# Kernel tuning notes

Measured on AMD Instinct MI355X. Metric: run time of the kernel, lower is better.

The kernel has to match this reference:

```python
import jax, jax.numpy as jnp
import numpy as np

N, E, T = 50000, 800000, 12
H, HEADS, L, O = 128, 4, 3, 12
C = H // HEADS
NEG_SLOPE = 0.2
LN_EPS = 1e-5


def setup_inputs() -> dict:
    key = jax.random.key(0)
    ks = iter(jax.random.split(key, 32))
    rn = lambda shape, s=0.1: jax.random.normal(next(ks), shape, jnp.float32) * s
    return {
        "x": rn((N, T), 1.0),
        "edge_index": jax.random.randint(next(ks), (2, E), 0, N, dtype=jnp.int32),
        "edge_attr": jax.random.uniform(next(ks), (E, 1), jnp.float32),
        "gru_Wih0": rn((3 * H, 1)), "gru_Whh0": rn((3 * H, H)),
        "gru_bih0": rn((3 * H,)), "gru_bhh0": rn((3 * H,)),
        "gru_Wih1": rn((3 * H, H)), "gru_Whh1": rn((3 * H, H)),
        "gru_bih1": rn((3 * H,)), "gru_bhh1": rn((3 * H,)),
        "gat_Wl": rn((L, H, H)), "gat_bl": rn((L, H)),
        "gat_Wr": rn((L, H, H)), "gat_br": rn((L, H)),
        "gat_We": rn((L, 1, H)),
        "gat_att": rn((L, HEADS, C)),
        "gat_bias": rn((L, H)),
        "ln_gamma": jnp.ones((L, H), jnp.float32),
        "ln_beta": jnp.zeros((L, H), jnp.float32),
        "fc_W1": rn((H, H)), "fc_b1": rn((H,)),
        "fc_W2": rn((H, O)), "fc_b2": rn((O,)),
    }


def _gru_layer(xs, Wih, Whh, bih, bhh):
    # xs: [T, N, D] time-major. Standard torch GRU cell math.
    gx = jnp.einsum('tnd,gd->tng', xs, Wih) + bih  # [T, N, 3H]
    h0 = jnp.zeros((xs.shape[1], H), xs.dtype)

    def step(h, g):
        gh = h @ Whh.T + bhh
        r = jax.nn.sigmoid(g[:, :H] + gh[:, :H])
        z = jax.nn.sigmoid(g[:, H:2 * H] + gh[:, H:2 * H])
        n = jnp.tanh(g[:, 2 * H:] + r * gh[:, 2 * H:])
        h_new = (1.0 - z) * n + z * h
        return h_new, h_new

    hT, hs = jax.lax.scan(step, h0, gx)
    return hT, hs


def _gatv2(x, src, dst, edge_attr, Wl, bl, Wr, br, We, att, bias):
    # GATv2Conv with edge features, no self loops, concat heads.
    xl = (x @ Wl + bl).reshape(N, HEADS, C)   # source transform (x_j)
    xr = (x @ Wr + br).reshape(N, HEADS, C)   # target transform (x_i)
    ee = (edge_attr @ We).reshape(-1, HEADS, C)
    m = xl[src] + xr[dst] + ee                # [E, HEADS, C]
    s = jnp.sum(jax.nn.leaky_relu(m, NEG_SLOPE) * att, axis=-1)  # [E, HEADS]
    smax = jax.lax.stop_gradient(jax.ops.segment_max(s, dst, num_segments=N))
    es = jnp.exp(s - smax[dst])
    denom = jax.ops.segment_sum(es, dst, num_segments=N)
    alpha = es / jnp.maximum(denom[dst], 1e-16)
    out = jax.ops.segment_sum(alpha[:, :, None] * xl[src], dst, num_segments=N)
    return out.reshape(N, H) + bias


def _layernorm(x, g, b):
    mu = jnp.mean(x, -1, keepdims=True)
    var = jnp.var(x, -1, keepdims=True)
    return (x - mu) * jax.lax.rsqrt(var + LN_EPS) * g + b


def _forward(x, edge_index, edge_attr,
             gru_Wih0, gru_Whh0, gru_bih0, gru_bhh0,
             gru_Wih1, gru_Whh1, gru_bih1, gru_bhh1,
             gat_Wl, gat_bl, gat_Wr, gat_br, gat_We, gat_att, gat_bias,
             ln_gamma, ln_beta, fc_W1, fc_b1, fc_W2, fc_b2):
    # Temporal: 2-layer GRU over the window, take final hidden of top layer.
    xs = x.T[:, :, None]                                  # [T, N, 1]
    _, hs0 = _gru_layer(xs, gru_Wih0, gru_Whh0, gru_bih0, gru_bhh0)
    h, _ = _gru_layer(hs0, gru_Wih1, gru_Whh1, gru_bih1, gru_bhh1)  # [N, H]

    src, dst = edge_index[0], edge_index[1]
    for l in range(L):
        res = h
        z = _gatv2(h, src, dst, edge_attr,
                   gat_Wl[l], gat_bl[l], gat_Wr[l], gat_br[l],
                   gat_We[l], gat_att[l], gat_bias[l])
        z = _layernorm(z, ln_gamma[l], ln_beta[l])
        h = jax.nn.elu(z) + res                           # dropout off (eval)

    h1 = jax.nn.relu(h @ fc_W1 + fc_b1)
    return h1 @ fc_W2 + fc_b2                             # [N, O]


def reference(x, edge_index, edge_attr,
              gru_Wih0, gru_Whh0, gru_bih0, gru_bhh0,
              gru_Wih1, gru_Whh1, gru_bih1, gru_bhh1,
              gat_Wl, gat_bl, gat_Wr, gat_br, gat_We, gat_att, gat_bias,
              ln_gamma, ln_beta, fc_W1, fc_b1, fc_W2, fc_b2):
    return _forward(x, edge_index, edge_attr,
                    gru_Wih0, gru_Whh0, gru_bih0, gru_bhh0,
                    gru_Wih1, gru_Whh1, gru_bih1, gru_bhh1,
                    gat_Wl, gat_bl, gat_Wr, gat_br, gat_We, gat_att, gat_bias,
                    ln_gamma, ln_beta, fc_W1, fc_b1, fc_W2, fc_b2)
```

## Files before the change

### kernel.cpp

```cpp
#include <hip/hip_runtime.h>

#define NN 50000
#define EE 800000
#define TT 12
#define HH 128
#define LLAYERS 3
#define OO 12

typedef __attribute__((ext_vector_type(8))) short short8;
typedef __attribute__((ext_vector_type(4))) float float4v;
typedef unsigned short ushort_t;

#define MFMA_BF16 __builtin_amdgcn_mfma_f32_16x16x32_bf16

#define L2E  1.4426950408889634f
#define L2E2 2.8853900817779268f

#if __has_builtin(__builtin_amdgcn_exp2f)
#define EXP2(x) __builtin_amdgcn_exp2f(x)
#else
#define EXP2(x) __expf((x) * 0.6931471805599453f)
#endif

__device__ __forceinline__ ushort_t f2b(float f) {
    union { float f; unsigned u; } v; v.f = f;
    unsigned u = v.u;
    return (ushort_t)((u + 0x7FFFu + ((u >> 16) & 1u)) >> 16);
}
__device__ __forceinline__ float b2f(ushort_t b) {
    union { unsigned u; float f; } v; v.u = ((unsigned)b) << 16; return v.f;
}
__device__ __forceinline__ short8 ld8(const ushort_t* p) { return *(const short8*)p; }

__device__ __forceinline__ float rcpf_(float x) { return __builtin_amdgcn_rcpf(x); }
__device__ __forceinline__ float sig2(float y) { return rcpf_(1.f + EXP2(-y)); }
__device__ __forceinline__ float tanh2(float y) {
    return fmaf(2.f, rcpf_(1.f + EXP2(-y)), -1.f);
}

__device__ __forceinline__ short8 lds_frag(const ushort_t* tile, int row, int kb) {
    int off = (row << 8) + kb;
    off ^= (row & 7) << 4;
    return *(const short8*)((const char*)tile + off);
}
__device__ __forceinline__ void lds_wr16(ushort_t* tile, int row, int cb, ushort_t v) {
    int off = (row << 8) + cb;
    off ^= (row & 7) << 4;
    *(ushort_t*)((char*)tile + off) = v;
}

__global__ __launch_bounds__(512, 2)
void gru_all(const float* __restrict__ x,
             const ushort_t* __restrict__ Whh0b, const float* __restrict__ Wih0,
             const float* __restrict__ bih0, const float* __restrict__ bhh0,
             const ushort_t* __restrict__ Wih1b, const ushort_t* __restrict__ Whh1b,
             const float* __restrict__ bih1, const float* __restrict__ bhh1,
             float* __restrict__ h1f, ushort_t* __restrict__ h1b) {
    __shared__ ushort_t h0sA[4608], h0sB[4608], h1sA[4608], h1sB[4608];
    __shared__ float xsh[384];

    const int tid = threadIdx.x;
    const int wv = tid >> 6, lane = tid & 63;
    const int cl = lane & 15, kg = lane >> 4;
    const int r0 = blockIdx.x * 32;
    const int jj = wv * 16 + cl;

    short8 w0[3][4], wxx[3][4], whh[3][4];
#pragma unroll
    for (int g = 0; g < 3; ++g)
#pragma unroll
        for (int ks = 0; ks < 4; ++ks) {
            const size_t ro = (size_t)(g * 128 + jj) * HH + ks * 32 + kg * 8;
            w0[g][ks]  = ld8(Whh0b + ro);
            wxx[g][ks] = ld8(Wih1b + ro);
            whh[g][ks] = ld8(Whh1b + ro);
        }
    const float wiR = Wih0[jj] * L2E, wiZ = Wih0[jj + 128] * L2E, wiN = Wih0[jj + 256] * L2E2;
    const float b0R = (bih0[jj] + bhh0[jj]) * L2E;
    const float b0Z = (bih0[jj + 128] + bhh0[jj + 128]) * L2E;
    const float b0N = bih0[jj + 256] * L2E2;
    const float c0N = bhh0[jj + 256] * L2E2;
    const float b1R = (bih1[jj] + bhh1[jj]) * L2E;
    const float b1Z = (bih1[jj + 128] + bhh1[jj + 128]) * L2E;
    const float b1N = bih1[jj + 256] * L2E2;
    const float c1N = bhh1[jj + 256] * L2E2;

    const int rdl = kg * 288 + cl * 16;
    const int ksw = jj >> 5;
    const int kcw = (jj >> 3) & 3;
    const int wbase = (ksw * 8 + kcw) * 288 + kg * 64 + (jj & 7) * 2;

    for (int q = tid; q < 384; q += 512) {
        int row = q / 12, tt = q - row * 12;
        int node = r0 + row;
        xsh[q] = (node < NN) ? x[(size_t)node * TT + tt] : 0.f;
    }
    for (int q = tid; q < 2304; q += 512) {
        ((unsigned*)h0sA)[q] = 0u; ((unsigned*)h0sB)[q] = 0u;
        ((unsigned*)h1sA)[q] = 0u; ((unsigned*)h1sB)[q] = 0u;
    }
    float h0r[2][4] = {}; float h1r[2][4] = {};
    __syncthreads();

    ushort_t* h0c = h0sA; ushort_t* h0n = h0sB;
    ushort_t* h1c = h1sA; ushort_t* h1n = h1sB;

#pragma unroll 1
    for (int t = 0; t < TT; ++t) {
#pragma unroll
        for (int rt = 0; rt < 2; ++rt) {
            short8 a[4];
#pragma unroll
            for (int ks = 0; ks < 4; ++ks)
                a[ks] = *(const short8*)((const char*)h0c + ks * 2304 + rt * 1152 + rdl);
            float4v aR = {0,0,0,0}, aZ = {0,0,0,0}, aN = {0,0,0,0};
#pragma unroll
            for (int ks = 0; ks < 4; ++ks) {
                aR = MFMA_BF16(a[ks], w0[0][ks], aR, 0, 0, 0);
                aZ = MFMA_BF16(a[ks], w0[1][ks], aZ, 0, 0, 0);
                aN = MFMA_BF16(a[ks], w0[2][ks], aN, 0, 0, 0);
            }
#pragma unroll
            for (int i = 0; i < 4; ++i) {
                const int rl = rt * 16 + kg * 4 + i;
                float xv = xsh[rl * 12 + t];
                float hold = h0r[rt][i];
                float r = sig2(fmaf(xv, wiR, b0R) + aR[i]);
                float z = sig2(fmaf(xv, wiZ, b0Z) + aZ[i]);
                float nn2 = tanh2(fmaf(xv, wiN, b0N) + r * (aN[i] + c0N));
                float hn = fmaf(z, hold - nn2, nn2);
                h0r[rt][i] = hn;
                *(ushort_t*)((char*)h0n + wbase + rt * 1152 + i * 16) = f2b(hn);
            }
        }
        __syncthreads();
#pragma unroll
        for (int rt = 0; rt < 2; ++rt) {
            short8 an[4], a1[4];
#pragma unroll
            for (int ks = 0; ks < 4; ++ks) {
                an[ks] = *(const short8*)((const char*)h0n + ks * 2304 + rt * 1152 + rdl);
                a1[ks] = *(const short8*)((const char*)h1c + ks * 2304 + rt * 1152 + rdl);
            }
            float4v gR = {0,0,0,0}, gZ = {0,0,0,0}, xN = {0,0,0,0}, hN = {0,0,0,0};
#pragma unroll
            for (int ks = 0; ks < 4; ++ks) {
                gR = MFMA_BF16(an[ks], wxx[0][ks], gR, 0, 0, 0);
                gZ = MFMA_BF16(an[ks], wxx[1][ks], gZ, 0, 0, 0);
                xN = MFMA_BF16(an[ks], wxx[2][ks], xN, 0, 0, 0);
                gR = MFMA_BF16(a1[ks], whh[0][ks], gR, 0, 0, 0);
                gZ = MFMA_BF16(a1[ks], whh[1][ks], gZ, 0, 0, 0);
                hN = MFMA_BF16(a1[ks], whh[2][ks], hN, 0, 0, 0);
            }
#pragma unroll
            for (int i = 0; i < 4; ++i) {
                float hold = h1r[rt][i];
                float r = sig2(gR[i] + b1R);
                float z = sig2(gZ[i] + b1Z);
                float nn2 = tanh2(xN[i] + b1N + r * (hN[i] + c1N));
                float hn = fmaf(z, hold - nn2, nn2);
                h1r[rt][i] = hn;
                *(ushort_t*)((char*)h1n + wbase + rt * 1152 + i * 16) = f2b(hn);
            }
        }
        __syncthreads();
        ushort_t* tmp0 = h0c; h0c = h0n; h0n = tmp0;
        ushort_t* tmp1 = h1c; h1c = h1n; h1n = tmp1;
    }

#pragma unroll
    for (int rt = 0; rt < 2; ++rt)
#pragma unroll
        for (int i = 0; i < 4; ++i) {
            int node = r0 + rt * 16 + kg * 4 + i;
            if (node < NN) {
                float v = h1r[rt][i];
                const size_t off = (size_t)node * HH + jj;
                h1f[off] = v;
                h1b[off] = f2b(v);
            }
        }
}

__global__ __launch_bounds__(256)
void gemm_dual(const ushort_t* __restrict__ A,
               const ushort_t* __restrict__ B1, const ushort_t* __restrict__ B2,
               const float* __restrict__ bias1, const float* __restrict__ bias2,
               ushort_t* __restrict__ C1, ushort_t* __restrict__ C2) {
    const int wave = threadIdx.x >> 6, lane = threadIdx.x & 63;
    const int r0 = (blockIdx.x * 4 + wave) * 16;
    const int col = lane & 15, kg = lane >> 4;
    const int arow = min(r0 + col, NN - 1);
    short8 a[4];
#pragma unroll
    for (int ks = 0; ks < 4; ++ks)
        a[ks] = ld8(A + (size_t)arow * HH + ks * 32 + kg * 8);
#pragma unroll
    for (int j0 = 0; j0 < 8; ++j0) {
        float4v c1 = {0,0,0,0}, c2 = {0,0,0,0};
        const ushort_t* p1 = B1 + (size_t)(j0 * 16 + col) * HH + kg * 8;
        const ushort_t* p2 = B2 + (size_t)(j0 * 16 + col) * HH + kg * 8;
#pragma unroll
        for (int ks = 0; ks < 4; ++ks) {
            c1 = MFMA_BF16(a[ks], ld8(p1 + ks * 32), c1, 0, 0, 0);
            c2 = MFMA_BF16(a[ks], ld8(p2 + ks * 32), c2, 0, 0, 0);
        }
        const int jj = j0 * 16 + col;
        const float b1 = bias1[jj], b2 = bias2[jj];
#pragma unroll
        for (int i = 0; i < 4; ++i) {
            int node = r0 + kg * 4 + i;
            if (node >= NN) continue;
            C1[(size_t)node * HH + jj] = f2b(c1[i] + b1);
            C2[(size_t)node * HH + jj] = f2b(c2[i] + b2);
        }
    }
}

__global__ void csr_count(const int* __restrict__ dst, int* __restrict__ deg) {
    int e = blockIdx.x * 256 + threadIdx.x;
    if (e < EE) atomicAdd(&deg[dst[e]], 1);
}

__global__ void csr_alloc(const int* __restrict__ deg, int* __restrict__ rowbeg,
                          int* __restrict__ cursor, int* __restrict__ gcnt) {
    int n = blockIdx.x * 256 + threadIdx.x;
    int ln = threadIdx.x & 63;
    int d = (n < NN) ? deg[n] : 0;
    int s = d;
#pragma unroll
    for (int off = 1; off < 64; off <<= 1) {
        int t = __shfl_up(s, off);
        if (ln >= off) s += t;
    }
    int base = 0;
    if (ln == 63) base = atomicAdd(gcnt, s);
    base = __shfl(base, 63);
    int excl = base + s - d;
    if (n < NN) { rowbeg[n] = excl; cursor[n] = excl; }
}

__global__ void csr_fill(const int* __restrict__ src, const int* __restrict__ dst,
                         const float* __restrict__ ea, int* __restrict__ cursor,
                         int* __restrict__ srcS, float* __restrict__ eaS) {
    int e = blockIdx.x * 256 + threadIdx.x;
    if (e >= EE) return;
    int pos = atomicAdd(&cursor[dst[e]], 1);
    srcS[pos] = src[e];
    eaS[pos] = ea[e];
}

__global__ __launch_bounds__(256)
void gat_fused(const int* __restrict__ rowbeg, const int* __restrict__ deg,
               const int* __restrict__ srcS, const float* __restrict__ eaS,
               const ushort_t* __restrict__ xlb, const ushort_t* __restrict__ xrb,
               const float* __restrict__ We, const float* __restrict__ att,
               const float* __restrict__ gbias, const float* __restrict__ gamma,
               const float* __restrict__ beta,
               float* __restrict__ h1f, ushort_t* __restrict__ h1b) {
    const int node = (blockIdx.x * 256 + threadIdx.x) >> 6;
    const int lane = threadIdx.x & 63;
    if (node >= NN) return;
    const int g = lane >> 4, gl = lane & 15;
    const int cb = gl * 8;

    short8 xrv = ld8(xrb + (size_t)node * HH + cb);
    float xr[8], Wv[8], Av[8];
#pragma unroll
    for (int c = 0; c < 8; ++c) xr[c] = b2f((ushort_t)xrv[c]);
    *(float4*)&Wv[0] = *(const float4*)(We + cb);
    *(float4*)&Wv[4] = *(const float4*)(We + cb + 4);
    *(float4*)&Av[0] = *(const float4*)(att + cb);
    *(float4*)&Av[4] = *(const float4*)(att + cb + 4);

    const int beg = rowbeg[node];
    const int end = beg + deg[node];
    float acc[8] = {};
    float den = 0.f;

    for (int base = beg; base < end; base += 4) {
        int eslot = base + g;
        bool valid = eslot < end;
        int es = valid ? eslot : end - 1;
        int sN = srcS[es];
        float ev = eaS[es];
        short8 xlv = ld8(xlb + (size_t)sN * HH + cb);
        float xl[8];
        float p = 0.f;
#pragma unroll
        for (int c = 0; c < 8; ++c) {
            xl[c] = b2f((ushort_t)xlv[c]);
            float m = xl[c] + xr[c] + ev * Wv[c];
            m = (m > 0.f) ? m : 0.2f * m;
            p = fmaf(m, Av[c], p);
        }
        p += __shfl_xor(p, 1);
        p += __shfl_xor(p, 2);
        float w = valid ? __expf(p) : 0.f;
        den += w;
#pragma unroll
        for (int c = 0; c < 8; ++c) acc[c] = fmaf(w, xl[c], acc[c]);
    }
#pragma unroll
    for (int c = 0; c < 8; ++c) {
        acc[c] += __shfl_xor(acc[c], 16);
        acc[c] += __shfl_xor(acc[c], 32);
    }
    den += __shfl_xor(den, 16);
    den += __shfl_xor(den, 32);

    float invd = 1.f / fmaxf(den, 1e-16f);
    float gb[8];
    *(float4*)&gb[0] = *(const float4*)(gbias + cb);
    *(float4*)&gb[4] = *(const float4*)(gbias + cb + 4);
    float o[8], s1 = 0.f, s2 = 0.f;
#pragma unroll
    for (int c = 0; c < 8; ++c) {
        o[c] = acc[c] * invd + gb[c];
        s1 += o[c];
        s2 = fmaf(o[c], o[c], s2);
    }
#pragma unroll
    for (int d = 1; d < 16; d <<= 1) {
        s1 += __shfl_xor(s1, d);
        s2 += __shfl_xor(s2, d);
    }
    float mean = s1 * (1.f / 128.f);
    float var = s2 * (1.f / 128.f) - mean * mean;
    float inv = rsqrtf(var + 1e-5f);

    if (g == 0) {
        float gm[8], bt[8], hv[8];
        *(float4*)&gm[0] = *(const float4*)(gamma + cb);
        *(float4*)&gm[4] = *(const float4*)(gamma + cb + 4);
        *(float4*)&bt[0] = *(const float4*)(beta + cb);
        *(float4*)&bt[4] = *(const float4*)(beta + cb + 4);
        *(float4*)&hv[0] = *(const float4*)(h1f + (size_t)node * HH + cb);
        *(float4*)&hv[4] = *(const float4*)(h1f + (size_t)node * HH + cb + 4);
        short8 pk;
#pragma unroll
        for (int c = 0; c < 8; ++c) {
            float y = (o[c] - mean) * inv * gm[c] + bt[c];
            y = (y > 0.f) ? y : expm1f(y);
            hv[c] += y;
            pk[c] = (short)f2b(hv[c]);
        }
        *(float4*)(h1f + (size_t)node * HH + cb)     = *(float4*)&hv[0];
        *(float4*)(h1f + (size_t)node * HH + cb + 4) = *(float4*)&hv[4];
        *(short8*)(h1b + (size_t)node * HH + cb) = pk;
    }
}

__global__ __launch_bounds__(256)
void fc_head(const ushort_t* __restrict__ A, const ushort_t* __restrict__ W1b,
             const float* __restrict__ b1, const ushort_t* __restrict__ W2b,
             const float* __restrict__ b2, float* __restrict__ out) {
    __shared__ ushort_t hs[4][2048];
    const int wave = threadIdx.x >> 6, lane = threadIdx.x & 63;
    const int r0 = (blockIdx.x * 4 + wave) * 16;
    const int col = lane & 15, kg = lane >> 4;
    const int arow = min(r0 + col, NN - 1);
    short8 a[4];
#pragma unroll
    for (int ks = 0; ks < 4; ++ks)
        a[ks] = ld8(A + (size_t)arow * HH + ks * 32 + kg * 8);
#pragma unroll
    for (int j0 = 0; j0 < 8; ++j0) {
        float4v acc = {0,0,0,0};
        const ushort_t* bp = W1b + (size_t)(j0 * 16 + col) * HH + kg * 8;
#pragma unroll
        for (int ks = 0; ks < 4; ++ks)
            acc = MFMA_BF16(a[ks], ld8(bp + ks * 32), acc, 0, 0, 0);
        const int jj = j0 * 16 + col;
        const float bj = b1[jj];
#pragma unroll
        for (int i = 0; i < 4; ++i)
            lds_wr16(hs[wave], kg * 4 + i, jj * 2, f2b(fmaxf(acc[i] + bj, 0.f)));
    }
    short8 f[4];
#pragma unroll
    for (int ks = 0; ks < 4; ++ks)
        f[ks] = lds_frag(hs[wave], col, ks * 64 + kg * 16);
    float4v acc2 = {0,0,0,0};
#pragma unroll
    for (int ks = 0; ks < 4; ++ks)
        acc2 = MFMA_BF16(f[ks], ld8(W2b + (size_t)col * HH + ks * 32 + kg * 8), acc2, 0, 0, 0);
    if (col < OO) {
        const float bj = b2[col];
#pragma unroll
        for (int i = 0; i < 4; ++i) {
            int node = r0 + kg * 4 + i;
            if (node < NN) out[(size_t)node * OO + col] = acc2[i] + bj;
        }
    }
}

__global__ void conv_all(const float* __restrict__ Whh0, const float* __restrict__ Wih1,
                         const float* __restrict__ Whh1, const float* __restrict__ gWl,
                         const float* __restrict__ gWr, const float* __restrict__ fcW1,
                         const float* __restrict__ fcW2,
                         ushort_t* __restrict__ Whh0b, ushort_t* __restrict__ Wih1b,
                         ushort_t* __restrict__ Whh1b, ushort_t* __restrict__ WlTb,
                         ushort_t* __restrict__ WrTb, ushort_t* __restrict__ W1Tb,
                         ushort_t* __restrict__ W2Tb) {
    int idx = blockIdx.x * 256 + threadIdx.x;
    if (idx < 147456) {
        const float* s; ushort_t* d; int o = idx;
        if (o < 49152)        { s = Whh0; d = Whh0b; }
        else if (o < 98304)   { s = Wih1; d = Wih1b; o -= 49152; }
        else                  { s = Whh1; d = Whh1b; o -= 98304; }
        float scale = (o >= 256 * 128) ? L2E2 : L2E;
        d[o] = f2b(s[o] * scale);
    } else if (idx < 262144) {
        int local = idx - 147456;
        int mt = local >> 14, o = local & 16383;
        int r = o >> 7, c = o & 127;
        const float* s; ushort_t* d;
        if (mt < 3)      { s = gWl + (size_t)mt * 16384;       d = WlTb + (size_t)mt * 16384; }
        else if (mt < 6) { s = gWr + (size_t)(mt - 3) * 16384; d = WrTb + (size_t)(mt - 3) * 16384; }
        else             { s = fcW1;                            d = W1Tb; }
        d[c * 128 + r] = f2b(s[r * 128 + c]);
    } else if (idx < 264192) {
        int o = idx - 262144;
        int j = o >> 7, k = o & 127;
        W2Tb[o] = (j < OO) ? f2b(fcW2[k * OO + j]) : (ushort_t)0;
    }
}

extern "C" void kernel_launch(void* const* d_in, const int* in_sizes, int n_in,
                              void* d_out, int out_size, void* d_ws, size_t ws_size,
                              hipStream_t stream) {
    const float* x     = (const float*)d_in[0];
    const int*   ei    = (const int*)d_in[1];
    const int*   src   = ei;
    const int*   dst   = ei + EE;
    const float* ea    = (const float*)d_in[2];
    const float* Wih0  = (const float*)d_in[3];
    const float* Whh0  = (const float*)d_in[4];
    const float* bih0  = (const float*)d_in[5];
    const float* bhh0  = (const float*)d_in[6];
    const float* Wih1  = (const float*)d_in[7];
    const float* Whh1  = (const float*)d_in[8];
    const float* bih1  = (const float*)d_in[9];
    const float* bhh1  = (const float*)d_in[10];
    const float* gWl   = (const float*)d_in[11];
    const float* gbl   = (const float*)d_in[12];
    const float* gWr   = (const float*)d_in[13];
    const float* gbr   = (const float*)d_in[14];
    const float* gWe   = (const float*)d_in[15];
    const float* gatt  = (const float*)d_in[16];
    const float* gbias = (const float*)d_in[17];
    const float* lng   = (const float*)d_in[18];
    const float* lnb   = (const float*)d_in[19];
    const float* fcW1  = (const float*)d_in[20];
    const float* fcb1  = (const float*)d_in[21];
    const float* fcW2  = (const float*)d_in[22];
    const float* fcb2  = (const float*)d_in[23];
    float* out = (float*)d_out;
    float* ws  = (float*)d_ws;

    const size_t NH = (size_t)NN * HH;

    ushort_t* h1b   = (ushort_t*)ws;
    ushort_t* xlb   = h1b + NH;
    ushort_t* xrb   = xlb + NH;
    ushort_t* Whh0b = xrb + NH;
    ushort_t* Wih1b = Whh0b + 49152;
    ushort_t* Whh1b = Wih1b + 49152;
    ushort_t* WlTb  = Whh1b + 49152;
    ushort_t* WrTb  = WlTb + 49152;
    ushort_t* W1Tb  = WrTb + 49152;
    ushort_t* W2Tb  = W1Tb + 16384;

    float* p    = ws + (3 * NH + 5 * 49152 + 16384 + 2048) / 2;
    float* h1f  = p; p += NH;
    int* deg    = (int*)p;
    int* rowbeg = deg + NN;
    int* cursor = rowbeg + NN;
    int* gcnt   = cursor + NN;
    int* srcS   = gcnt + 4;
    float* eaS  = (float*)(srcS + EE);

    conv_all<<<1032, 256, 0, stream>>>(Whh0, Wih1, Whh1, gWl, gWr, fcW1, fcW2,
                                       Whh0b, Wih1b, Whh1b, WlTb, WrTb, W1Tb, W2Tb);

    hipMemsetAsync(deg, 0, (size_t)NN * sizeof(int), stream);
    hipMemsetAsync(gcnt, 0, 4 * sizeof(int), stream);
    csr_count<<<(EE + 255) / 256, 256, 0, stream>>>(dst, deg);
    csr_alloc<<<(NN + 255) / 256, 256, 0, stream>>>(deg, rowbeg, cursor, gcnt);
    csr_fill<<<(EE + 255) / 256, 256, 0, stream>>>(src, dst, ea, cursor, srcS, eaS);

    gru_all<<<(NN + 31) / 32, 512, 0, stream>>>(x, Whh0b, Wih0, bih0, bhh0,
                                                Wih1b, Whh1b, bih1, bhh1, h1f, h1b);

    const int rowBlocks = (NN + 63) / 64;
    const int fusedBlocks = (NN + 3) / 4;
    for (int l = 0; l < LLAYERS; ++l) {
        gemm_dual<<<rowBlocks, 256, 0, stream>>>(h1b, WlTb + (size_t)l * 16384,
                                                 WrTb + (size_t)l * 16384,
                                                 gbl + l * HH, gbr + l * HH, xlb, xrb);
        gat_fused<<<fusedBlocks, 256, 0, stream>>>(rowbeg, deg, srcS, eaS, xlb, xrb,
                                                   gWe + l * HH, gatt + l * HH,
                                                   gbias + l * HH, lng + l * HH, lnb + l * HH,
                                                   h1f, h1b);
    }

    fc_head<<<rowBlocks, 256, 0, stream>>>(h1b, W1Tb, fcb1, W2Tb, fcb2, out);
}
```

Before: 731.0 us.

## Enlarge GRU and GEMM row tiles and prefetch next edge gather in GAT

The GRU kernel now handles 64 rows per block and keeps hidden state in fp32 shared memory instead of registers. The dual GEMM and FC head process 32 rows per wave so each weight fragment feeds two MFMAs. The GAT aggregation loop prefetches the next edge's source feature and attribute while computing the current edge. The larger GRU shared memory footprint reduces the number of resident blocks per CU and adds LDS traffic for the state.

```diff
diff --git a/kernel.cpp b/kernel.cpp
--- a/kernel.cpp
+++ b/kernel.cpp
@@ -48,6 +48,8 @@
     off ^= (row & 7) << 4;
     *(ushort_t*)((char*)tile + off) = v;
 }
+
+#define MSTRIDE 132
 
 __global__ __launch_bounds__(512, 2)
 void gru_all(const float* __restrict__ x,
@@ -56,13 +58,14 @@
              const ushort_t* __restrict__ Wih1b, const ushort_t* __restrict__ Whh1b,
              const float* __restrict__ bih1, const float* __restrict__ bhh1,
              float* __restrict__ h1f, ushort_t* __restrict__ h1b) {
-    __shared__ ushort_t h0sA[4608], h0sB[4608], h1sA[4608], h1sB[4608];
-    __shared__ float xsh[384];
+    __shared__ ushort_t h0sA[9216], h0sB[9216], h1sA[9216], h1sB[9216];
+    __shared__ float h0m[64 * MSTRIDE], h1m[64 * MSTRIDE];
+    __shared__ float xsh[768];
 
     const int tid = threadIdx.x;
     const int wv = tid >> 6, lane = tid & 63;
     const int cl = lane & 15, kg = lane >> 4;
-    const int r0 = blockIdx.x * 32;
+    const int r0 = blockIdx.x * 64;
     const int jj = wv * 16 + cl;
 
     short8 w0[3][4], wxx[3][4], whh[3][4];
@@ -88,18 +91,17 @@
     const int rdl = kg * 288 + cl * 16;
     const int ksw = jj >> 5;
     const int kcw = (jj >> 3) & 3;
-    const int wbase = (ksw * 8 + kcw) * 288 + kg * 64 + (jj & 7) * 2;
-
-    for (int q = tid; q < 384; q += 512) {
+    const int wbase = (ksw * 16 + kcw) * 288 + kg * 64 + (jj & 7) * 2;
+
+    for (int q = tid; q < 768; q += 512) {
         int row = q / 12, tt = q - row * 12;
         int node = r0 + row;
         xsh[q] = (node < NN) ? x[(size_t)node * TT + tt] : 0.f;
     }
-    for (int q = tid; q < 2304; q += 512) {
-        ((unsigned*)h0sA)[q] = 0u; ((unsigned*)h0sB)[q] = 0u;
-        ((unsigned*)h1sA)[q] = 0u; ((unsigned*)h1sB)[q] = 0u;
-    }
-    float h0r[2][4] = {}; float h1r[2][4] = {};
+    for (int q = tid; q < 4608; q += 512) {
+        ((unsigned*)h0sA)[q] = 0u; ((unsigned*)h1sA)[q] = 0u;
+    }
+    for (int q = tid; q < 64 * MSTRIDE; q += 512) { h0m[q] = 0.f; h1m[q] = 0.f; }
     __syncthreads();
 
     ushort_t* h0c = h0sA; ushort_t* h0n = h0sB;
@@ -107,12 +109,12 @@
 
 #pragma unroll 1
     for (int t = 0; t < TT; ++t) {
-#pragma unroll
-        for (int rt = 0; rt < 2; ++rt) {
+#pragma unroll 1
+        for (int rt = 0; rt < 4; ++rt) {
             short8 a[4];
 #pragma unroll
             for (int ks = 0; ks < 4; ++ks)
-                a[ks] = *(const short8*)((const char*)h0c + ks * 2304 + rt * 1152 + rdl);
+                a[ks] = *(const short8*)((const char*)h0c + ks * 4608 + rt * 1152 + rdl);
             float4v aR = {0,0,0,0}, aZ = {0,0,0,0}, aN = {0,0,0,0};
 #pragma unroll
             for (int ks = 0; ks < 4; ++ks) {
@@ -124,23 +126,23 @@
             for (int i = 0; i < 4; ++i) {
                 const int rl = rt * 16 + kg * 4 + i;
                 float xv = xsh[rl * 12 + t];
-                float hold = h0r[rt][i];
+                float hold = h0m[rl * MSTRIDE + jj];
                 float r = sig2(fmaf(xv, wiR, b0R) + aR[i]);
                 float z = sig2(fmaf(xv, wiZ, b0Z) + aZ[i]);
                 float nn2 = tanh2(fmaf(xv, wiN, b0N) + r * (aN[i] + c0N));
                 float hn = fmaf(z, hold - nn2, nn2);
-                h0r[rt][i] = hn;
+                h0m[rl * MSTRIDE + jj] = hn;
                 *(ushort_t*)((char*)h0n + wbase + rt * 1152 + i * 16) = f2b(hn);
             }
         }
         __syncthreads();
-#pragma unroll
-        for (int rt = 0; rt < 2; ++rt) {
+#pragma unroll 1
+        for (int rt = 0; rt < 4; ++rt) {
             short8 an[4], a1[4];
 #pragma unroll
             for (int ks = 0; ks < 4; ++ks) {
-                an[ks] = *(const short8*)((const char*)h0n + ks * 2304 + rt * 1152 + rdl);
-                a1[ks] = *(const short8*)((const char*)h1c + ks * 2304 + rt * 1152 + rdl);
+                an[ks] = *(const short8*)((const char*)h0n + ks * 4608 + rt * 1152 + rdl);
+                a1[ks] = *(const short8*)((const char*)h1c + ks * 4608 + rt * 1152 + rdl);
             }
             float4v gR = {0,0,0,0}, gZ = {0,0,0,0}, xN = {0,0,0,0}, hN = {0,0,0,0};
 #pragma unroll
@@ -154,12 +156,13 @@
             }
 #pragma unroll
             for (int i = 0; i < 4; ++i) {
-                float hold = h1r[rt][i];
+                const int rl = rt * 16 + kg * 4 + i;
+                float hold = h1m[rl * MSTRIDE + jj];
                 float r = sig2(gR[i] + b1R);
                 float z = sig2(gZ[i] + b1Z);
                 float nn2 = tanh2(xN[i] + b1N + r * (hN[i] + c1N));
                 float hn = fmaf(z, hold - nn2, nn2);
-                h1r[rt][i] = hn;
+                h1m[rl * MSTRIDE + jj] = hn;
                 *(ushort_t*)((char*)h1n + wbase + rt * 1152 + i * 16) = f2b(hn);
             }
         }
@@ -169,12 +172,13 @@
     }
 
 #pragma unroll
-    for (int rt = 0; rt < 2; ++rt)
+    for (int rt = 0; rt < 4; ++rt)
 #pragma unroll
         for (int i = 0; i < 4; ++i) {
-            int node = r0 + rt * 16 + kg * 4 + i;
+            const int rl = rt * 16 + kg * 4 + i;
+            int node = r0 + rl;
             if (node < NN) {
-                float v = h1r[rt][i];
+                float v = h1m[rl * MSTRIDE + jj];
                 const size_t off = (size_t)node * HH + jj;
                 h1f[off] = v;
                 h1b[off] = f2b(v);
@@ -188,31 +192,44 @@
                const float* __restrict__ bias1, const float* __restrict__ bias2,
                ushort_t* __restrict__ C1, ushort_t* __restrict__ C2) {
     const int wave = threadIdx.x >> 6, lane = threadIdx.x & 63;
-    const int r0 = (blockIdx.x * 4 + wave) * 16;
+    const int r0 = (blockIdx.x * 4 + wave) * 32;
     const int col = lane & 15, kg = lane >> 4;
-    const int arow = min(r0 + col, NN - 1);
-    short8 a[4];
-#pragma unroll
-    for (int ks = 0; ks < 4; ++ks)
-        a[ks] = ld8(A + (size_t)arow * HH + ks * 32 + kg * 8);
+    const int arow0 = min(r0 + col, NN - 1);
+    const int arow1 = min(r0 + 16 + col, NN - 1);
+    short8 a0[4], a1[4];
+#pragma unroll
+    for (int ks = 0; ks < 4; ++ks) {
+        a0[ks] = ld8(A + (size_t)arow0 * HH + ks * 32 + kg * 8);
+        a1[ks] = ld8(A + (size_t)arow1 * HH + ks * 32 + kg * 8);
+    }
 #pragma unroll
     for (int j0 = 0; j0 < 8; ++j0) {
-        float4v c1 = {0,0,0,0}, c2 = {0,0,0,0};
+        float4v c10 = {0,0,0,0}, c11 = {0,0,0,0}, c20 = {0,0,0,0}, c21 = {0,0,0,0};
         const ushort_t* p1 = B1 + (size_t)(j0 * 16 + col) * HH + kg * 8;
         const ushort_t* p2 = B2 + (size_t)(j0 * 16 + col) * HH + kg * 8;
 #pragma unroll
         for (int ks = 0; ks < 4; ++ks) {
-            c1 = MFMA_BF16(a[ks], ld8(p1 + ks * 32), c1, 0, 0, 0);
-            c2 = MFMA_BF16(a[ks], ld8(p2 + ks * 32), c2, 0, 0, 0);
+            short8 b1v = ld8(p1 + ks * 32);
+            short8 b2v = ld8(p2 + ks * 32);
+            c10 = MFMA_BF16(a0[ks], b1v, c10, 0, 0, 0);
+            c11 = MFMA_BF16(a1[ks], b1v, c11, 0, 0, 0);
+            c20 = MFMA_BF16(a0[ks], b2v, c20, 0, 0, 0);
+            c21 = MFMA_BF16(a1[ks], b2v, c21, 0, 0, 0);
         }
         const int jj = j0 * 16 + col;
         const float b1 = bias1[jj], b2 = bias2[jj];
 #pragma unroll
         for (int i = 0; i < 4; ++i) {
-            int node = r0 + kg * 4 + i;
-            if (node >= NN) continue;
-            C1[(size_t)node * HH + jj] = f2b(c1[i] + b1);
-            C2[(size_t)node * HH + jj] = f2b(c2[i] + b2);
+            int node0 = r0 + kg * 4 + i;
+            int node1 = node0 + 16;
+            if (node0 < NN) {
+                C1[(size_t)node0 * HH + jj] = f2b(c10[i] + b1);
+                C2[(size_t)node0 * HH + jj] = f2b(c20[i] + b2);
+            }
+            if (node1 < NN) {
+                C1[(size_t)node1 * HH + jj] = f2b(c11[i] + b1);
+                C2[(size_t)node1 * HH + jj] = f2b(c21[i] + b2);
+            }
         }
     }
 }
@@ -278,28 +295,38 @@
     float acc[8] = {};
     float den = 0.f;
 
-    for (int base = beg; base < end; base += 4) {
-        int eslot = base + g;
-        bool valid = eslot < end;
-        int es = valid ? eslot : end - 1;
-        int sN = srcS[es];
+    if (beg < end) {
+        bool valid = (beg + g) < end;
+        int es = min(beg + g, end - 1);
         float ev = eaS[es];
-        short8 xlv = ld8(xlb + (size_t)sN * HH + cb);
-        float xl[8];
-        float p = 0.f;
-#pragma unroll
-        for (int c = 0; c < 8; ++c) {
-            xl[c] = b2f((ushort_t)xlv[c]);
-            float m = xl[c] + xr[c] + ev * Wv[c];
-            m = (m > 0.f) ? m : 0.2f * m;
-            p = fmaf(m, Av[c], p);
-        }
-        p += __shfl_xor(p, 1);
-        p += __shfl_xor(p, 2);
-        float w = valid ? __expf(p) : 0.f;
-        den += w;
-#pragma unroll
-        for (int c = 0; c < 8; ++c) acc[c] = fmaf(w, xl[c], acc[c]);
+        short8 xlv = ld8(xlb + (size_t)srcS[es] * HH + cb);
+        for (int base = beg; base < end; base += 4) {
+            int nbase = base + 4;
+            float ev2 = 0.f; short8 xlv2 = {};
+            bool nvalid = false;
+            if (nbase < end) {
+                nvalid = (nbase + g) < end;
+                int nes = min(nbase + g, end - 1);
+                ev2 = eaS[nes];
+                xlv2 = ld8(xlb + (size_t)srcS[nes] * HH + cb);
+            }
+            float xl[8];
+            float p = 0.f;
+#pragma unroll
+            for (int c = 0; c < 8; ++c) {
+                xl[c] = b2f((ushort_t)xlv[c]);
+                float m = xl[c] + xr[c] + ev * Wv[c];
+                m = (m > 0.f) ? m : 0.2f * m;
+                p = fmaf(m, Av[c], p);
+            }
+            p += __shfl_xor(p, 1);
+            p += __shfl_xor(p, 2);
+            float w = valid ? __expf(p) : 0.f;
+            den += w;
+#pragma unroll
+            for (int c = 0; c < 8; ++c) acc[c] = fmaf(w, xl[c], acc[c]);
+            valid = nvalid; ev = ev2; xlv = xlv2;
+        }
     }
 #pragma unroll
     for (int c = 0; c < 8; ++c) {
@@ -355,42 +382,57 @@
 void fc_head(const ushort_t* __restrict__ A, const ushort_t* __restrict__ W1b,
              const float* __restrict__ b1, const ushort_t* __restrict__ W2b,
              const float* __restrict__ b2, float* __restrict__ out) {
-    __shared__ ushort_t hs[4][2048];
+    __shared__ ushort_t hs[4][4096];
     const int wave = threadIdx.x >> 6, lane = threadIdx.x & 63;
-    const int r0 = (blockIdx.x * 4 + wave) * 16;
+    const int r0 = (blockIdx.x * 4 + wave) * 32;
     const int col = lane & 15, kg = lane >> 4;
-    const int arow = min(r0 + col, NN - 1);
-    short8 a[4];
-#pragma unroll
-    for (int ks = 0; ks < 4; ++ks)
-        a[ks] = ld8(A + (size_t)arow * HH + ks * 32 + kg * 8);
+    const int arow0 = min(r0 + col, NN - 1);
+    const int arow1 = min(r0 + 16 + col, NN - 1);
+    short8 a0[4], a1[4];
+#pragma unroll
+    for (int ks = 0; ks < 4; ++ks) {
+        a0[ks] = ld8(A + (size_t)arow0 * HH + ks * 32 + kg * 8);
+        a1[ks] = ld8(A + (size_t)arow1 * HH + ks * 32 + kg * 8);
+    }
 #pragma unroll
     for (int j0 = 0; j0 < 8; ++j0) {
-        float4v acc = {0,0,0,0};
+        float4v acc0 = {0,0,0,0}, acc1 = {0,0,0,0};
         const ushort_t* bp = W1b + (size_t)(j0 * 16 + col) * HH + kg * 8;
 #pragma unroll
-        for (int ks = 0; ks < 4; ++ks)
-            acc = MFMA_BF16(a[ks], ld8(bp + ks * 32), acc, 0, 0, 0);
+        for (int ks = 0; ks < 4; ++ks) {
+            short8 bv = ld8(bp + ks * 32);
+            acc0 = MFMA_BF16(a0[ks], bv, acc0, 0, 0, 0);
+            acc1 = MFMA_BF16(a1[ks], bv, acc1, 0, 0, 0);
+        }
         const int jj = j0 * 16 + col;
         const float bj = b1[jj];
 #pragma unroll
-        for (int i = 0; i < 4; ++i)
-            lds_wr16(hs[wave], kg * 4 + i, jj * 2, f2b(fmaxf(acc[i] + bj, 0.f)));
-    }
-    short8 f[4];
+        for (int i = 0; i < 4; ++i) {
+            lds_wr16(hs[wave], kg * 4 + i, jj * 2, f2b(fmaxf(acc0[i] + bj, 0.f)));
+            lds_wr16(hs[wave], 16 + kg * 4 + i, jj * 2, f2b(fmaxf(acc1[i] + bj, 0.f)));
+        }
+    }
+    short8 w2f[4];
 #pragma unroll
     for (int ks = 0; ks < 4; ++ks)
-        f[ks] = lds_frag(hs[wave], col, ks * 64 + kg * 16);
-    float4v acc2 = {0,0,0,0};
-#pragma unroll
-    for (int ks = 0; ks < 4; ++ks)
-        acc2 = MFMA_BF16(f[ks], ld8(W2b + (size_t)col * HH + ks * 32 + kg * 8), acc2, 0, 0, 0);
-    if (col < OO) {
-        const float bj = b2[col];
-#pragma unroll
-        for (int i = 0; i < 4; ++i) {
-            int node = r0 + kg * 4 + i;
-            if (node < NN) out[(size_t)node * OO + col] = acc2[i] + bj;
+        w2f[ks] = ld8(W2b + (size_t)col * HH + ks * 32 + kg * 8);
+#pragma unroll
+    for (int rh = 0; rh < 2; ++rh) {
+        short8 f[4];
+#pragma unroll
+        for (int ks = 0; ks < 4; ++ks)
+            f[ks] = lds_frag(hs[wave], rh * 16 + col, ks * 64 + kg * 16);
+        float4v acc2 = {0,0,0,0};
+#pragma unroll
+        for (int ks = 0; ks < 4; ++ks)
+            acc2 = MFMA_BF16(f[ks], w2f[ks], acc2, 0, 0, 0);
+        if (col < OO) {
+            const float bj = b2[col];
+#pragma unroll
+            for (int i = 0; i < 4; ++i) {
+                int node = r0 + rh * 16 + kg * 4 + i;
+                if (node < NN) out[(size_t)node * OO + col] = acc2[i] + bj;
+            }
         }
     }
 }
@@ -490,20 +532,20 @@
     csr_alloc<<<(NN + 255) / 256, 256, 0, stream>>>(deg, rowbeg, cursor, gcnt);
     csr_fill<<<(EE + 255) / 256, 256, 0, stream>>>(src, dst, ea, cursor, srcS, eaS);
 
-    gru_all<<<(NN + 31) / 32, 512, 0, stream>>>(x, Whh0b, Wih0, bih0, bhh0,
+    gru_all<<<(NN + 63) / 64, 512, 0, stream>>>(x, Whh0b, Wih0, bih0, bhh0,
                                                 Wih1b, Whh1b, bih1, bhh1, h1f, h1b);
 
-    const int rowBlocks = (NN + 63) / 64;
+    const int dualBlocks = (NN + 127) / 128;
     const int fusedBlocks = (NN + 3) / 4;
     for (int l = 0; l < LLAYERS; ++l) {
-        gemm_dual<<<rowBlocks, 256, 0, stream>>>(h1b, WlTb + (size_t)l * 16384,
-                                                 WrTb + (size_t)l * 16384,
-                                                 gbl + l * HH, gbr + l * HH, xlb, xrb);
+        gemm_dual<<<dualBlocks, 256, 0, stream>>>(h1b, WlTb + (size_t)l * 16384,
+                                                  WrTb + (size_t)l * 16384,
+                                                  gbl + l * HH, gbr + l * HH, xlb, xrb);
         gat_fused<<<fusedBlocks, 256, 0, stream>>>(rowbeg, deg, srcS, eaS, xlb, xrb,
                                                    gWe + l * HH, gatt + l * HH,
                                                    gbias + l * HH, lng + l * HH, lnb + l * HH,
                                                    h1f, h1b);
     }
 
-    fc_head<<<rowBlocks, 256, 0, stream>>>(h1b, W1Tb, fcb1, W2Tb, fcb2, out);
-}
+    fc_head<<<dualBlocks, 256, 0, stream>>>(h1b, W1Tb, fcb1, W2Tb, fcb2, out);
+}
```

Result: faster. 680.7 us (-6.9%).
